# Kernel optimization log

Hardware: AMD Instinct MI355X
Metric: run time of the kernel (lower is better)

The kernel has to match this reference:

```python
import jax, jax.numpy as jnp
import numpy as np

L, H, C, T, V = 6, 12, 768, 1024, 50257
HD = C // H
B = 2
EPS = 1e-5


def setup_inputs() -> dict:
    key = jax.random.key(0)
    ks = jax.random.split(key, 10)
    std = 0.02
    proj_std = 0.02 / np.sqrt(2 * L)  # specialized init for projection layers

    def n(k, shape, s=std):
        return jax.random.normal(k, shape, dtype=jnp.float32) * s

    return {
        "tokens": jax.random.randint(ks[0], (B, T), 0, V),
        "tok_emb": n(ks[1], (V, C)),
        "pos_emb": n(ks[2], (T, C)),
        # per-layer stacked params, leading dim L (scanned)
        "Wq": n(ks[3], (L, H, C, HD)),
        "Wk": n(ks[4], (L, H, C, HD)),
        "Wv": n(ks[5], (L, H, C, HD)),
        "Wo": n(ks[6], (L, C, C), proj_std),
        "bo": jnp.zeros((L, C), jnp.float32),
        "ln1_g": jnp.ones((L, C), jnp.float32),
        "ln1_b": jnp.zeros((L, C), jnp.float32),
        "ln2_g": jnp.ones((L, C), jnp.float32),
        "ln2_b": jnp.zeros((L, C), jnp.float32),
        "W1": n(ks[7], (L, C, 4 * C)),
        "b1": jnp.zeros((L, 4 * C), jnp.float32),
        "W2": n(ks[8], (L, 4 * C, C), proj_std),
        "b2": jnp.zeros((L, C), jnp.float32),
        "lnf_g": jnp.ones((C,), jnp.float32),
        "lnf_b": jnp.zeros((C,), jnp.float32),
        "head_w": n(ks[9], (C, V)),
        "head_b": jnp.zeros((V,), jnp.float32),
    }


def _ln(x, g, b):
    m = x.mean(-1, keepdims=True)
    v = ((x - m) ** 2).mean(-1, keepdims=True)
    return (x - m) * jax.lax.rsqrt(v + EPS) * g + b


def _forward(tokens, p):
    x = p["tok_emb"][tokens] + p["pos_emb"][None, : tokens.shape[1]]  # [B,T,C]
    mask = jnp.tril(jnp.ones((T, T), dtype=bool))
    scale = C ** -0.5  # NOTE: original scales by input channel C, not head_size

    def block(x, lp):
        Wq, Wk, Wv, Wo, bo, g1, b1, g2, b2, W1, bb1, W2, bb2 = lp
        # NOTE: original writes x = ln1(x); x = x + attn(x)  (residual from normed x)
        x = _ln(x, g1, b1)
        q = jnp.einsum("btc,hcd->bhtd", x, Wq)
        k = jnp.einsum("btc,hcd->bhtd", x, Wk)
        v = jnp.einsum("btc,hcd->bhtd", x, Wv)
        s = jnp.einsum("bhtd,bhsd->bhts", q, k) * scale
        s = jnp.where(mask, s, -jnp.inf)
        a = jax.nn.softmax(s, axis=-1)
        y = jnp.einsum("bhts,bhsd->bhtd", a, v)
        y = y.transpose(0, 2, 1, 3).reshape(x.shape)  # concat heads -> [B,T,C]
        x = x + y @ Wo + bo
        x = _ln(x, g2, b2)
        h = jax.nn.gelu(x @ W1 + bb1, approximate=False)  # torch GELU = exact erf
        x = x + h @ W2 + bb2
        return x, None

    lps = (p["Wq"], p["Wk"], p["Wv"], p["Wo"], p["bo"], p["ln1_g"], p["ln1_b"],
           p["ln2_g"], p["ln2_b"], p["W1"], p["b1"], p["W2"], p["b2"])
    x, _ = jax.lax.scan(block, x, lps)
    x = _ln(x, p["lnf_g"], p["lnf_b"])
    return x @ p["head_w"] + p["head_b"]  # [B,T,V]


def reference(tokens, tok_emb, pos_emb, Wq, Wk, Wv, Wo, bo, ln1_g, ln1_b,
              ln2_g, ln2_b, W1, b1, W2, b2, lnf_g, lnf_b, head_w, head_b):
    p = dict(tok_emb=tok_emb, pos_emb=pos_emb, Wq=Wq, Wk=Wk, Wv=Wv, Wo=Wo, bo=bo,
             ln1_g=ln1_g, ln1_b=ln1_b, ln2_g=ln2_g, ln2_b=ln2_b, W1=W1, b1=b1,
             W2=W2, b2=b2, lnf_g=lnf_g, lnf_b=lnf_b, head_w=head_w, head_b=head_b)
    return _forward(tokens, p)
```

## Files before the change

### kernel.cpp

```cpp
#include <hip/hip_runtime.h>
#include <hip/hip_bf16.h>
#include <stdint.h>
#include <math.h>


#define L_ 6
#define H_ 12
#define C_ 768
#define T_ 1024
#define V_ 50257
#define VP2_ 50432
#define HD_ 64
#define BT_ 2048
#define F_ 3072
#define SCALE_ 0.03608439182435161f
#define NEGBIG_ -1e30f

typedef __bf16 bf;
typedef __attribute__((ext_vector_type(8))) __bf16 bf16x8;
typedef __attribute__((ext_vector_type(4))) __bf16 bf16x4;
typedef __attribute__((ext_vector_type(4))) float f32x4;

__device__ __forceinline__ void gload16(const void* g, void* l) {
  __builtin_amdgcn_global_load_lds(
      (const __attribute__((address_space(1))) unsigned int*)g,
      (__attribute__((address_space(3))) unsigned int*)l, 16, 0, 0);
}

__device__ __forceinline__ float gelu_f(float x) {
  return 0.5f * x * (1.0f + erff(x * 0.70710678118654752f));
}

__global__ __launch_bounds__(256) void embed_k(const int* __restrict__ tok,
                                               const float* __restrict__ te,
                                               const float* __restrict__ pe,
                                               float* __restrict__ x) {
  int bt = blockIdx.x;
  int c = blockIdx.y * 256 + threadIdx.x;
  int t = bt & (T_ - 1);
  int v = tok[bt];
  x[(size_t)bt * C_ + c] = te[(size_t)v * C_ + c] + pe[(size_t)t * C_ + c];
}

__global__ __launch_bounds__(256) void ln_k(const float* __restrict__ xin,
                                            float* __restrict__ xout,
                                            bf* __restrict__ xb,
                                            const float* __restrict__ g,
                                            const float* __restrict__ b) {
  int row = blockIdx.x;
  const float* xr = xin + (size_t)row * C_;
  int tid = threadIdx.x;
  float v0 = xr[tid], v1 = xr[tid + 256], v2 = xr[tid + 512];
  float s1 = v0 + v1 + v2;
  float s2 = v0 * v0 + v1 * v1 + v2 * v2;
#pragma unroll
  for (int o = 32; o > 0; o >>= 1) {
    s1 += __shfl_xor(s1, o, 64);
    s2 += __shfl_xor(s2, o, 64);
  }
  __shared__ float r1[4], r2[4];
  int w = tid >> 6, lane = tid & 63;
  if (lane == 0) { r1[w] = s1; r2[w] = s2; }
  __syncthreads();
  float S1 = r1[0] + r1[1] + r1[2] + r1[3];
  float S2 = r2[0] + r2[1] + r2[2] + r2[3];
  float mean = S1 * (1.0f / C_);
  float var = S2 * (1.0f / C_) - mean * mean;
  float rs = rsqrtf(fmaxf(var, 0.0f) + 1e-5f);
  float* xo = xout + (size_t)row * C_;
  bf* xbo = xb + (size_t)row * C_;
  float vv[3] = {v0, v1, v2};
#pragma unroll
  for (int j = 0; j < 3; ++j) {
    int c = tid + j * 256;
    float o = (vv[j] - mean) * rs * g[c] + b[c];
    xo[c] = o;
    xbo[c] = (bf)o;
  }
}

__device__ __forceinline__ void transpose_body(const float* __restrict__ src,
                                               bf* __restrict__ dst, int src_ld,
                                               int dst_ld, int k0, int n0,
                                               int nmax) {
  __shared__ __align__(16) bf tl[64][72];
  int tid = threadIdx.x;
  int r = tid >> 2;
  int cb = (tid & 3) * 16;
#pragma unroll
  for (int j4 = 0; j4 < 4; ++j4) {
    int c = cb + j4 * 4;
    int n = n0 + c;
    size_t idx = (size_t)(k0 + r) * src_ld + n;
    const float* sp = src + idx;
    if (n + 4 <= nmax && (idx & 3) == 0) {
      f32x4 v = *(const f32x4*)sp;
      tl[r][c] = (bf)v[0];
      tl[r][c + 1] = (bf)v[1];
      tl[r][c + 2] = (bf)v[2];
      tl[r][c + 3] = (bf)v[3];
    } else {
#pragma unroll
      for (int j = 0; j < 4; ++j)
        tl[r][c + j] = (n + j < nmax) ? (bf)sp[j] : (bf)0.0f;
    }
  }
  __syncthreads();
  int n = n0 + r;
  bf16x8 w0, w1;
#pragma unroll
  for (int j = 0; j < 8; ++j) {
    w0[j] = tl[cb + j][r];
    w1[j] = tl[cb + 8 + j][r];
  }
  bf* dp = dst + (size_t)n * dst_ld + k0 + cb;
  *(bf16x8*)dp = w0;
  *(bf16x8*)(dp + 8) = w1;
}

__global__ __launch_bounds__(256) void transpose_k(const float* __restrict__ src,
                                                   bf* __restrict__ dst,
                                                   int src_ld, int dst_ld,
                                                   int nmax) {
  transpose_body(src, dst, src_ld, dst_ld, blockIdx.x * 64, blockIdx.y * 64,
                 nmax);
}

__global__ __launch_bounds__(256) void trans_layer_k(
    const float* __restrict__ Wq, const float* __restrict__ Wk,
    const float* __restrict__ Wv, const float* __restrict__ Wo,
    const float* __restrict__ W1, const float* __restrict__ W2,
    bf* __restrict__ wqkvT, bf* __restrict__ woT, bf* __restrict__ w1T,
    bf* __restrict__ w2T) {
  int r = blockIdx.x;
  if (r < 432) {
    int z = r / 12, k0 = (r % 12) * 64;
    int tsel = z / H_, hh = z % H_;
    const float* W = (tsel == 0) ? Wq : (tsel == 1) ? Wk : Wv;
    transpose_body(W + (size_t)hh * C_ * HD_,
                   wqkvT + (size_t)(tsel * C_ + hh * HD_) * C_, HD_, C_, k0, 0,
                   HD_);
  } else if (r < 576) {
    r -= 432;
    transpose_body(Wo, woT, C_, C_, (r % 12) * 64, (r / 12) * 64, C_);
  } else if (r < 1152) {
    r -= 576;
    transpose_body(W1, w1T, F_, C_, (r % 12) * 64, (r / 12) * 64, F_);
  } else {
    r -= 1152;
    transpose_body(W2, w2T, C_, F_, (r % 48) * 64, (r / 48) * 64, C_);
  }
}

template <int MODE, int BM, int BN, int NW, int KSPLIT>
__global__ __launch_bounds__(NW * 64) void gemm_bt(
    const bf* __restrict__ A, const bf* __restrict__ Bt,
    const float* __restrict__ bias, float* __restrict__ xres,
    bf* __restrict__ o0, bf* __restrict__ o1, bf* __restrict__ o2, int K) {
  constexpr int WM = BM / 2;
  constexpr int WN = BN / (NW / 2);
  constexpr int MI = WM / 16, NJ = WN / 16;
  constexpr int HALF = (BM + BN) * 64;
  __shared__ __align__(16) bf smem[2 * HALF];
  const int tid = threadIdx.x;
  const int w = tid >> 6, lane = tid & 63;
  const int wm = (NW == 8) ? (w >> 2) : (w >> 1);
  const int wn = (NW == 8) ? (w & 3) : (w & 1);
  const int lm = lane & 15, lg = lane >> 4;

  const int lin = blockIdx.y * gridDim.x + blockIdx.x;
  const int q8 = (gridDim.x * gridDim.y) >> 3;
  const int wg = (lin & 7) * q8 + (lin >> 3);
  const int mt = gridDim.y;
  const int m0 = (wg % mt) * BM, n0 = (wg / mt) * BN;

  const int kchunk = K / KSPLIT;
  const int kbase = (KSPLIT == 2) ? blockIdx.z * kchunk : 0;

  const int lr8 = lane >> 3;
  const int lc8s = ((lane & 7) ^ lr8) * 8;

  auto stage = [&](int buf, int k0) {
    bf* aL = smem + buf * HALF;
    bf* bL = aL + BM * 64;
#pragma unroll
    for (int c = 0; c < BM / (8 * NW); ++c) {
      int row = c * (8 * NW) + w * 8;
      gload16(A + (size_t)(m0 + row + lr8) * K + k0 + lc8s, &aL[row * 64]);
    }
#pragma unroll
    for (int c = 0; c < BN / (8 * NW); ++c) {
      int row = c * (8 * NW) + w * 8;
      gload16(Bt + (size_t)(n0 + row + lr8) * K + k0 + lc8s, &bL[row * 64]);
    }
  };

  f32x4 acc[MI][NJ];
#pragma unroll
  for (int i = 0; i < MI; ++i)
#pragma unroll
    for (int j = 0; j < NJ; ++j) acc[i][j] = (f32x4){0.f, 0.f, 0.f, 0.f};

  const int cXor = (lm & 7) * 8;
  const int NT = kchunk >> 6;
  stage(0, kbase);
  __syncthreads();
  int cur = 0;
  for (int t = 0; t < NT; ++t) {
    if (t + 1 < NT) stage(cur ^ 1, kbase + ((t + 1) << 6));
    const bf* aL = smem + cur * HALF;
    const bf* bL = aL + BM * 64;
#pragma unroll
    for (int ks = 0; ks < 2; ++ks) {
      const int cc = (ks * 32 + lg * 8) ^ cXor;
      bf16x8 af[MI], bfv[NJ];
#pragma unroll
      for (int i = 0; i < MI; ++i)
        af[i] = *(const bf16x8*)&aL[(wm * WM + i * 16 + lm) * 64 + cc];
#pragma unroll
      for (int j = 0; j < NJ; ++j)
        bfv[j] = *(const bf16x8*)&bL[(wn * WN + j * 16 + lm) * 64 + cc];
      __builtin_amdgcn_s_setprio(1);
#pragma unroll
      for (int i = 0; i < MI; ++i)
#pragma unroll
        for (int j = 0; j < NJ; ++j)
          acc[i][j] = __builtin_amdgcn_mfma_f32_16x16x32_bf16(
              af[i], bfv[j], acc[i][j], 0, 0, 0);
      __builtin_amdgcn_s_setprio(0);
    }
    __syncthreads();
    cur ^= 1;
  }

  if constexpr (MODE == 3) {
    int ngj[NJ];
    float bv[NJ];
#pragma unroll
    for (int j = 0; j < NJ; ++j) {
      ngj[j] = n0 + wn * WN + j * 16 + lm;
      bv[j] = (ngj[j] < V_) ? bias[ngj[j]] : 0.f;
    }
#pragma unroll
    for (int i = 0; i < MI; ++i)
#pragma unroll
      for (int r = 0; r < 4; ++r) {
        int row = m0 + wm * WM + i * 16 + lg * 4 + r;
        float* orow = xres + (size_t)row * V_;
#pragma unroll
        for (int j = 0; j < NJ; ++j)
          if (ngj[j] < V_) orow[ngj[j]] = acc[i][j][r] + bv[j];
      }
    return;
  }

  if constexpr (MODE == 0) {
    const int bb = m0 >> 10;
    if (n0 >= 2 * C_) {
      bf* sv = smem;
#pragma unroll
      for (int i = 0; i < MI; ++i)
#pragma unroll
        for (int j = 0; j < NJ; ++j) {
          int dl = wn * WN + j * 16 + lm;
#pragma unroll
          for (int r = 0; r < 4; ++r) {
            int tl = wm * WM + i * 16 + lg * 4 + r;
            sv[dl * (BM + 8) + tl] = (bf)acc[i][j][r];
          }
        }
      __syncthreads();
      int dd_l = tid >> 1, half = tid & 1;
      size_t vrow = (size_t)bb * C_ + (n0 - 2 * C_) + dd_l;
      int t_base = m0 & (T_ - 1);
#pragma unroll
      for (int s = 0; s < 4; ++s) {
        int tt = half * 32 + s * 8;
        *(bf16x8*)(o2 + vrow * T_ + t_base + tt) =
            *(const bf16x8*)&sv[dd_l * (BM + 8) + tt];
      }
      return;
    }
    bf* dst = (n0 < C_) ? o0 : o1;
    int nb = (n0 < C_) ? n0 : n0 - C_;
    size_t basej[NJ];
#pragma unroll
    for (int j = 0; j < NJ; ++j) {
      int rr = nb + wn * WN + j * 16 + lm;
      int hh = rr >> 6, dd = rr & 63;
      basej[j] = ((size_t)(bb * H_ + hh) * T_) * HD_ + dd;
    }
#pragma unroll
    for (int i = 0; i < MI; ++i)
#pragma unroll
      for (int r = 0; r < 4; ++r) {
        int tt = (m0 + wm * WM + i * 16 + lg * 4 + r) & (T_ - 1);
#pragma unroll
        for (int j = 0; j < NJ; ++j)
          dst[basej[j] + (size_t)tt * HD_] = (bf)acc[i][j][r];
      }
    return;
  }

  int ngj[NJ];
  float bv[NJ];
#pragma unroll
  for (int j = 0; j < NJ; ++j) {
    ngj[j] = n0 + wn * WN + j * 16 + lm;
    bv[j] = (KSPLIT == 1 || blockIdx.z == 0) ? bias[ngj[j]] : 0.f;
  }
#pragma unroll
  for (int i = 0; i < MI; ++i)
#pragma unroll
    for (int r = 0; r < 4; ++r) {
      int row = m0 + wm * WM + i * 16 + lg * 4 + r;
      if constexpr (MODE == 1) {
        float* xrow = xres + (size_t)row * C_;
#pragma unroll
        for (int j = 0; j < NJ; ++j) {
          if constexpr (KSPLIT == 2)
            atomicAdd(&xrow[ngj[j]], acc[i][j][r] + bv[j]);
          else
            xrow[ngj[j]] += acc[i][j][r] + bv[j];
        }
      } else {
        bf* orow = o0 + (size_t)row * F_;
#pragma unroll
        for (int j = 0; j < NJ; ++j)
          orow[ngj[j]] = (bf)gelu_f(acc[i][j][r] + bv[j]);
      }
    }
}

__global__ __launch_bounds__(128) void attn_k(const bf* __restrict__ q,
                                              const bf* __restrict__ k,
                                              const bf* __restrict__ vt,
                                              bf* __restrict__ yb) {
  const int qb = blockIdx.x, bh = blockIdx.y;
  const int tid = threadIdx.x, w = tid >> 6, lane = tid & 63;
  const int lm = lane & 15, lg = lane >> 4;
  const int bb = bh / H_, hh = bh % H_;
  __shared__ __align__(16) bf kl[2][64 * 64];
  __shared__ __align__(16) bf vl[2][64 * 64];
  __shared__ __align__(16) bf pl[2][16 * 64];

  const int srcc = ((lane & 7) ^ (lane >> 3)) * 8;
  auto stage = [&](int buf, int kb) {
#pragma unroll
    for (int c = 0; c < 4; ++c) {
      int rbase = w * 32 + c * 8;
      gload16(k + ((size_t)bh * T_ + kb * 64 + rbase + (lane >> 3)) * HD_ +
                  srcc,
              &kl[buf][rbase * 64]);
      gload16(vt + ((size_t)bh * HD_ + rbase + (lane >> 3)) * T_ + kb * 64 +
                  srcc,
              &vl[buf][rbase * 64]);
    }
  };

  const int kx = lm & 7;

  const int qrow = qb * 32 + w * 16 + lm;
  const bf* qbase = q + ((size_t)bh * T_ + qrow) * HD_;
  bf16x8 qf0 = *(const bf16x8*)(qbase + lg * 8);
  bf16x8 qf1 = *(const bf16x8*)(qbase + 32 + lg * 8);

  f32x4 y[4];
#pragma unroll
  for (int i = 0; i < 4; ++i) y[i] = (f32x4){0.f, 0.f, 0.f, 0.f};
  float m_run = NEGBIG_, l_run = 0.f;

  const int kbmax = qb >> 1;
  stage(0, 0);
  __syncthreads();
  int cur = 0;
  for (int kb = 0; kb <= kbmax; ++kb) {
    if (kb < kbmax) stage(cur ^ 1, kb + 1);

    f32x4 s[4];
    __builtin_amdgcn_s_setprio(1);
#pragma unroll
    for (int t = 0; t < 4; ++t) {
      s[t] = (f32x4){0.f, 0.f, 0.f, 0.f};
      bf16x8 a0 =
          *(const bf16x8*)&kl[cur][(t * 16 + lm) * 64 + (lg ^ kx) * 8];
      s[t] = __builtin_amdgcn_mfma_f32_16x16x32_bf16(a0, qf0, s[t], 0, 0, 0);
      bf16x8 a1 =
          *(const bf16x8*)&kl[cur][(t * 16 + lm) * 64 + ((4 + lg) ^ kx) * 8];
      s[t] = __builtin_amdgcn_mfma_f32_16x16x32_bf16(a1, qf1, s[t], 0, 0, 0);
    }
    __builtin_amdgcn_s_setprio(0);

    float mx = NEGBIG_;
#pragma unroll
    for (int t = 0; t < 4; ++t)
#pragma unroll
      for (int r = 0; r < 4; ++r) {
        float v = s[t][r] * SCALE_;
        int kv = kb * 64 + t * 16 + lg * 4 + r;
        if (kv > qrow) v = NEGBIG_;
        s[t][r] = v;
        mx = fmaxf(mx, v);
      }
    mx = fmaxf(mx, __shfl_xor(mx, 16, 64));
    mx = fmaxf(mx, __shfl_xor(mx, 32, 64));
    float mnew = fmaxf(m_run, mx);
    float corr = __expf(m_run - mnew);
    float rs = 0.f;
#pragma unroll
    for (int t = 0; t < 4; ++t)
#pragma unroll
      for (int r = 0; r < 4; ++r) {
        float p = __expf(s[t][r] - mnew);
        s[t][r] = p;
        rs += p;
      }
    rs += __shfl_xor(rs, 16, 64);
    rs += __shfl_xor(rs, 32, 64);
    l_run = l_run * corr + rs;
    m_run = mnew;

#pragma unroll
    for (int t = 0; t < 4; ++t) {
      bf16x4 pk;
#pragma unroll
      for (int r = 0; r < 4; ++r) pk[r] = (bf)s[t][r];
      *(bf16x4*)&pl[w][lm * 64 + ((t * 16 + lg * 4) ^ (kx * 8))] = pk;
    }

    float cy0 = __shfl(corr, lg * 4 + 0, 64);
    float cy1 = __shfl(corr, lg * 4 + 1, 64);
    float cy2 = __shfl(corr, lg * 4 + 2, 64);
    float cy3 = __shfl(corr, lg * 4 + 3, 64);
#pragma unroll
    for (int nt = 0; nt < 4; ++nt) {
      y[nt][0] *= cy0;
      y[nt][1] *= cy1;
      y[nt][2] *= cy2;
      y[nt][3] *= cy3;
    }

    __builtin_amdgcn_s_setprio(1);
#pragma unroll
    for (int nt = 0; nt < 4; ++nt)
#pragma unroll
      for (int ks = 0; ks < 2; ++ks) {
        bf16x8 ap =
            *(const bf16x8*)&pl[w][lm * 64 + ((ks * 32 + lg * 8) ^ (kx * 8))];
        bf16x8 bv = *(const bf16x8*)&vl[cur][(nt * 16 + lm) * 64 +
                                             ((ks * 4 + lg) ^ kx) * 8];
        y[nt] = __builtin_amdgcn_mfma_f32_16x16x32_bf16(ap, bv, y[nt], 0, 0, 0);
      }
    __builtin_amdgcn_s_setprio(0);
    __syncthreads();
    cur ^= 1;
  }

  float ly[4];
#pragma unroll
  for (int r = 0; r < 4; ++r) ly[r] = __shfl(l_run, lg * 4 + r, 64);
#pragma unroll
  for (int nt = 0; nt < 4; ++nt) {
    int cc = hh * 64 + nt * 16 + lm;
#pragma unroll
    for (int r = 0; r < 4; ++r) {
      int qr = qb * 32 + w * 16 + lg * 4 + r;
      yb[((size_t)(bb * T_ + qr)) * C_ + cc] = (bf)(y[nt][r] / ly[r]);
    }
  }
}

extern "C" void kernel_launch(void* const* d_in, const int* in_sizes, int n_in,
                              void* d_out, int out_size, void* d_ws,
                              size_t ws_size, hipStream_t stream) {
  (void)in_sizes; (void)n_in; (void)out_size; (void)ws_size;
  const int* tokens = (const int*)d_in[0];
  const float* tok_emb = (const float*)d_in[1];
  const float* pos_emb = (const float*)d_in[2];
  const float* Wq = (const float*)d_in[3];
  const float* Wk = (const float*)d_in[4];
  const float* Wv = (const float*)d_in[5];
  const float* Wo = (const float*)d_in[6];
  const float* bo = (const float*)d_in[7];
  const float* ln1g = (const float*)d_in[8];
  const float* ln1b = (const float*)d_in[9];
  const float* ln2g = (const float*)d_in[10];
  const float* ln2b = (const float*)d_in[11];
  const float* W1 = (const float*)d_in[12];
  const float* b1 = (const float*)d_in[13];
  const float* W2 = (const float*)d_in[14];
  const float* b2 = (const float*)d_in[15];
  const float* lnfg = (const float*)d_in[16];
  const float* lnfb = (const float*)d_in[17];
  const float* headw = (const float*)d_in[18];
  const float* headb = (const float*)d_in[19];
  float* out = (float*)d_out;

  uint8_t* base = (uint8_t*)d_ws;
  size_t off = 0;
  auto alloc = [&](size_t n) -> uint8_t* {
    uint8_t* r = base + off;
    off += (n + 255) & ~(size_t)255;
    return r;
  };
  float* x = (float*)alloc((size_t)BT_ * C_ * 4);
  bf* xb = (bf*)alloc((size_t)BT_ * C_ * 2);
  bf* qq = (bf*)alloc((size_t)BT_ * C_ * 2);
  bf* kk = (bf*)alloc((size_t)BT_ * C_ * 2);
  bf* vt = (bf*)alloc((size_t)BT_ * C_ * 2);
  bf* ybuf = (bf*)alloc((size_t)BT_ * C_ * 2);
  bf* hb = (bf*)alloc((size_t)BT_ * F_ * 2);
  bf* wqkvT = (bf*)alloc((size_t)3 * C_ * C_ * 2);
  bf* woT = (bf*)alloc((size_t)C_ * C_ * 2);
  bf* w1T = (bf*)alloc((size_t)F_ * C_ * 2);
  bf* w2T = (bf*)alloc((size_t)C_ * F_ * 2);
  bf* headT = (bf*)alloc((size_t)VP2_ * C_ * 2);

  dim3 blk(256), blk8(512), blk2(128);
  transpose_k<<<dim3(C_ / 64, VP2_ / 64), blk, 0, stream>>>(headw, headT, V_,
                                                            C_, V_);
  embed_k<<<dim3(BT_, 3), blk, 0, stream>>>(tokens, tok_emb, pos_emb, x);

  for (int l = 0; l < L_; ++l) {
    trans_layer_k<<<1728, blk, 0, stream>>>(
        Wq + (size_t)l * H_ * C_ * HD_, Wk + (size_t)l * H_ * C_ * HD_,
        Wv + (size_t)l * H_ * C_ * HD_, Wo + (size_t)l * C_ * C_,
        W1 + (size_t)l * C_ * F_, W2 + (size_t)l * F_ * C_, wqkvT, woT, w1T,
        w2T);

    ln_k<<<BT_, blk, 0, stream>>>(x, x, xb, ln1g + l * C_, ln1b + l * C_);
    gemm_bt<0, 64, 128, 4, 1><<<dim3(2304 / 128, BT_ / 64), blk, 0, stream>>>(
        xb, wqkvT, nullptr, nullptr, qq, kk, vt, C_);
    attn_k<<<dim3(T_ / 32, 2 * H_), blk2, 0, stream>>>(qq, kk, vt, ybuf);
    gemm_bt<1, 64, 64, 4, 2>
        <<<dim3(C_ / 64, BT_ / 64, 2), blk, 0, stream>>>(
            ybuf, woT, bo + l * C_, x, nullptr, nullptr, nullptr, C_);
    ln_k<<<BT_, blk, 0, stream>>>(x, x, xb, ln2g + l * C_, ln2b + l * C_);
    gemm_bt<2, 128, 128, 8, 1>
        <<<dim3(F_ / 128, BT_ / 128), blk8, 0, stream>>>(
            xb, w1T, b1 + l * F_, nullptr, hb, nullptr, nullptr, C_);
    gemm_bt<1, 64, 64, 4, 2>
        <<<dim3(C_ / 64, BT_ / 64, 2), blk, 0, stream>>>(
            hb, w2T, b2 + l * C_, x, nullptr, nullptr, nullptr, F_);
  }

  ln_k<<<BT_, blk, 0, stream>>>(x, x, xb, lnfg, lnfb);
  gemm_bt<3, 256, 256, 8, 1><<<dim3(VP2_ / 256, BT_ / 256), blk8, 0, stream>>>(
      xb, headT, headb, out, nullptr, nullptr, nullptr, C_);
}
```

Before: 1.182 ms.

## Add triple-buffered GEMM pipeline and retile LM head GEMM to 256x128

Parameterizes the GEMM kernel with pipeline depth and wave layout, adding a three-stage LDS pipeline that uses explicit vmcnt waits and a single barrier per k-step instead of two syncthreads. The LM head GEMM now uses 256x128 tiles with a 4x2 wave grid and the triple buffer, aiming to hide global-load latency and improve occupancy or grid coverage. The other GEMMs keep their previous configuration. The hand-written vmcnt counts depend on the fixed number of loads per stage, which a static_assert guards.

```diff
diff --git a/kernel.cpp b/kernel.cpp
--- a/kernel.cpp
+++ b/kernel.cpp
@@ -152,20 +152,22 @@
   }
 }
 
-template <int MODE, int BM, int BN, int NW, int KSPLIT>
+template <int MODE, int BM, int BN, int NW, int KSPLIT, int DEPTH, int WAVE_M>
 __global__ __launch_bounds__(NW * 64) void gemm_bt(
     const bf* __restrict__ A, const bf* __restrict__ Bt,
     const float* __restrict__ bias, float* __restrict__ xres,
     bf* __restrict__ o0, bf* __restrict__ o1, bf* __restrict__ o2, int K) {
-  constexpr int WM = BM / 2;
-  constexpr int WN = BN / (NW / 2);
+  constexpr int WAVE_N = NW / WAVE_M;
+  constexpr int WM = BM / WAVE_M;
+  constexpr int WN = BN / WAVE_N;
   constexpr int MI = WM / 16, NJ = WN / 16;
   constexpr int HALF = (BM + BN) * 64;
-  __shared__ __align__(16) bf smem[2 * HALF];
+  constexpr int NBUF = (DEPTH == 3) ? 3 : 2;
+  __shared__ __align__(16) bf smem[NBUF * HALF];
   const int tid = threadIdx.x;
   const int w = tid >> 6, lane = tid & 63;
-  const int wm = (NW == 8) ? (w >> 2) : (w >> 1);
-  const int wn = (NW == 8) ? (w & 3) : (w & 1);
+  const int wm = w / WAVE_N;
+  const int wn = w % WAVE_N;
   const int lm = lane & 15, lg = lane >> 4;
 
   const int lin = blockIdx.y * gridDim.x + blockIdx.x;
@@ -203,13 +205,8 @@
 
   const int cXor = (lm & 7) * 8;
   const int NT = kchunk >> 6;
-  stage(0, kbase);
-  __syncthreads();
-  int cur = 0;
-  for (int t = 0; t < NT; ++t) {
-    if (t + 1 < NT) stage(cur ^ 1, kbase + ((t + 1) << 6));
-    const bf* aL = smem + cur * HALF;
-    const bf* bL = aL + BM * 64;
+
+  auto compute = [&](const bf* aL, const bf* bL) {
 #pragma unroll
     for (int ks = 0; ks < 2; ++ks) {
       const int cc = (ks * 32 + lg * 8) ^ cXor;
@@ -229,8 +226,34 @@
               af[i], bfv[j], acc[i][j], 0, 0, 0);
       __builtin_amdgcn_s_setprio(0);
     }
+  };
+
+  if constexpr (DEPTH == 3) {
+    static_assert((BM + BN) / (8 * NW) == 6, "vmcnt assumes 6 loads/stage");
+    stage(0, kbase);
+    if (NT > 1) stage(1, kbase + 64);
+    for (int t = 0; t < NT; ++t) {
+      if (t + 1 < NT)
+        asm volatile("s_waitcnt vmcnt(6)" ::: "memory");
+      else
+        asm volatile("s_waitcnt vmcnt(0)" ::: "memory");
+      __builtin_amdgcn_s_barrier();
+      __builtin_amdgcn_sched_barrier(0);
+      if (t + 2 < NT) stage((t + 2) % 3, kbase + ((t + 2) << 6));
+      const bf* aL = smem + (t % 3) * HALF;
+      compute(aL, aL + BM * 64);
+    }
+  } else {
+    stage(0, kbase);
     __syncthreads();
-    cur ^= 1;
+    int cur = 0;
+    for (int t = 0; t < NT; ++t) {
+      if (t + 1 < NT) stage(cur ^ 1, kbase + ((t + 1) << 6));
+      const bf* aL = smem + cur * HALF;
+      compute(aL, aL + BM * 64);
+      __syncthreads();
+      cur ^= 1;
+    }
   }
 
   if constexpr (MODE == 3) {
@@ -529,22 +552,24 @@
         w2T);
 
     ln_k<<<BT_, blk, 0, stream>>>(x, x, xb, ln1g + l * C_, ln1b + l * C_);
-    gemm_bt<0, 64, 128, 4, 1><<<dim3(2304 / 128, BT_ / 64), blk, 0, stream>>>(
-        xb, wqkvT, nullptr, nullptr, qq, kk, vt, C_);
+    gemm_bt<0, 64, 128, 4, 1, 1, 2>
+        <<<dim3(2304 / 128, BT_ / 64), blk, 0, stream>>>(
+            xb, wqkvT, nullptr, nullptr, qq, kk, vt, C_);
     attn_k<<<dim3(T_ / 32, 2 * H_), blk2, 0, stream>>>(qq, kk, vt, ybuf);
-    gemm_bt<1, 64, 64, 4, 2>
+    gemm_bt<1, 64, 64, 4, 2, 1, 2>
         <<<dim3(C_ / 64, BT_ / 64, 2), blk, 0, stream>>>(
             ybuf, woT, bo + l * C_, x, nullptr, nullptr, nullptr, C_);
     ln_k<<<BT_, blk, 0, stream>>>(x, x, xb, ln2g + l * C_, ln2b + l * C_);
-    gemm_bt<2, 128, 128, 8, 1>
+    gemm_bt<2, 128, 128, 8, 1, 1, 2>
         <<<dim3(F_ / 128, BT_ / 128), blk8, 0, stream>>>(
             xb, w1T, b1 + l * F_, nullptr, hb, nullptr, nullptr, C_);
-    gemm_bt<1, 64, 64, 4, 2>
+    gemm_bt<1, 64, 64, 4, 2, 1, 2>
         <<<dim3(C_ / 64, BT_ / 64, 2), blk, 0, stream>>>(
             hb, w2T, b2 + l * C_, x, nullptr, nullptr, nullptr, F_);
   }
 
   ln_k<<<BT_, blk, 0, stream>>>(x, x, xb, lnfg, lnfb);
-  gemm_bt<3, 256, 256, 8, 1><<<dim3(VP2_ / 256, BT_ / 256), blk8, 0, stream>>>(
-      xb, headT, headb, out, nullptr, nullptr, nullptr, C_);
-}
+  gemm_bt<3, 256, 128, 8, 1, 3, 4>
+      <<<dim3(VP2_ / 128, BT_ / 256), blk8, 0, stream>>>(
+          xb, headT, headb, out, nullptr, nullptr, nullptr, C_);
+}
```

After: 1.209 ms. +2.3%, slower.
